# Optimization experiments

Measured on AMD Instinct MI355X. Metric: run time of the kernel, lower is better.

Reference implementation:

```python
import jax, jax.numpy as jnp
import numpy as np

H = 768      # hidden_size (MambaConfig default)
DI = 500     # intermediate_size (overridden)
N = 16       # state_size
R = 48       # time_step_rank = ceil(768/16)
K = 4        # conv_kernel
LYR = 5      # num_hidden_layers
EPS = 1e-5   # layer_norm_epsilon
B, L, IN = 8, 1024, 4096


def _rmsnorm(x, w):
    v = jnp.mean(jnp.square(x), axis=-1, keepdims=True)
    return x * jax.lax.rsqrt(v + EPS) * w


def _mixer(x, in_proj, conv_w, conv_b, x_proj, dt_w, dt_b, A_log, Dp, out_w):
    # x: [B, L, H]
    proj = x @ in_proj                       # [B, L, 2*DI]
    u, gate = jnp.split(proj, 2, axis=-1)
    # causal depthwise conv1d (torch Conv1d padding=K-1, sliced to L)
    up = jnp.pad(u, ((0, 0), (K - 1, 0), (0, 0)))
    conv = conv_b
    for k in range(K):
        conv = conv + up[:, k:k + x.shape[1], :] * conv_w[:, k]
    u = jax.nn.silu(conv)                    # [B, L, DI]
    ssm = u @ x_proj                         # [B, L, R + 2N]
    dt, Bm, Cm = ssm[..., :R], ssm[..., R:R + N], ssm[..., R + N:]
    dt = jax.nn.softplus(dt @ dt_w + dt_b)   # [B, L, DI]
    A = -jnp.exp(A_log)                      # [DI, N]
    dA = jnp.exp(dt[..., None] * A)          # [B, L, DI, N]
    dBu = dt[..., None] * Bm[:, :, None, :] * u[..., None]  # [B, L, DI, N]

    def step(h, xs):
        dA_t, dBu_t, C_t = xs
        h = dA_t * h + dBu_t                 # [B, DI, N]
        y = jnp.einsum('bdn,bn->bd', h, C_t)
        return h, y

    h0 = jnp.zeros((u.shape[0], DI, N), dtype=u.dtype)
    _, ys = jax.lax.scan(step, h0, (dA.transpose(1, 0, 2, 3),
                                    dBu.transpose(1, 0, 2, 3),
                                    Cm.transpose(1, 0, 2)))
    y = ys.transpose(1, 0, 2)                # [B, L, DI]
    y = y + u * Dp
    y = y * jax.nn.silu(gate)
    return y @ out_w                         # [B, L, H]


def setup_inputs() -> dict:
    key = jax.random.key(0)
    ks = jax.random.split(key, 12)
    s = 0.02
    inputs = jax.random.normal(ks[0], (B, L, IN), jnp.float32)
    W_down = jax.random.normal(ks[1], (IN, H), jnp.float32) * s
    in_proj = jax.random.normal(ks[2], (LYR, H, 2 * DI), jnp.float32) * s
    conv_w = jax.random.normal(ks[3], (LYR, DI, K), jnp.float32) * 0.1
    conv_b = jnp.zeros((LYR, DI), jnp.float32)
    x_proj = jax.random.normal(ks[4], (LYR, DI, R + 2 * N), jnp.float32) * s
    dt_w = jax.random.normal(ks[5], (LYR, R, DI), jnp.float32) * s
    dt_b = jax.random.normal(ks[6], (LYR, DI), jnp.float32) * 0.1
    A_log = jnp.broadcast_to(jnp.log(jnp.arange(1, N + 1, dtype=jnp.float32)),
                             (LYR, DI, N)).copy()
    D_param = jnp.ones((LYR, DI), jnp.float32)
    out_w = jax.random.normal(ks[7], (LYR, DI, H), jnp.float32) * s
    norm_w = jnp.ones((LYR, H), jnp.float32)
    norm_f_w = jnp.ones((H,), jnp.float32)
    W_cls = jax.random.normal(ks[8], (H, 1), jnp.float32) * s
    return dict(inputs=inputs, W_down=W_down, in_proj=in_proj, conv_w=conv_w,
                conv_b=conv_b, x_proj=x_proj, dt_w=dt_w, dt_b=dt_b,
                A_log=A_log, D_param=D_param, out_w=out_w, norm_w=norm_w,
                norm_f_w=norm_f_w, W_cls=W_cls)


def reference(inputs, W_down, in_proj, conv_w, conv_b, x_proj, dt_w, dt_b,
              A_log, D_param, out_w, norm_w, norm_f_w, W_cls):
    x = inputs @ W_down                      # down projection [B, L, H]
    for i in range(LYR):
        x = x + _mixer(_rmsnorm(x, norm_w[i]), in_proj[i], conv_w[i],
                       conv_b[i], x_proj[i], dt_w[i], dt_b[i], A_log[i],
                       D_param[i], out_w[i])
    x = _rmsnorm(x, norm_f_w)
    out = x[:, -1]                           # last token [B, H]
    logits = out @ W_cls                     # [B, 1]
    return logits
```

## Files before the change

kernel.cpp:

```cpp
#include <hip/hip_runtime.h>
#include <hip/hip_bf16.h>

#define BATCH 8
#define SEQL 1024
#define INDIM 4096
#define HDIM 768
#define DI 500
#define NSTATE 16
#define RRANK 48
#define KCONV 4
#define NLAYER 5
#define BL (BATCH * SEQL)

typedef __attribute__((ext_vector_type(8))) short bf16x8;
typedef __attribute__((ext_vector_type(4))) float f32x4;

__device__ __forceinline__ void gl_lds16(const void* g, void* l) {
  __builtin_amdgcn_global_load_lds(
      (const __attribute__((address_space(1))) void*)g,
      (__attribute__((address_space(3))) void*)l, 16, 0, 0);
}

__device__ __forceinline__ unsigned short f2bf(float v) {
  return __hip_bfloat16_raw(__float2bfloat16(v)).x;
}
__device__ __forceinline__ float bf2f(unsigned short h) {
  unsigned int u = ((unsigned int)h) << 16;
  float f;
  memcpy(&f, &u, 4);
  return f;
}

template <int EPI>
__global__ __launch_bounds__(256) void gemm_mfma(
    const short* __restrict__ A, const short* __restrict__ Bt,
    float* __restrict__ C, const float* __restrict__ bias,
    unsigned short* __restrict__ D0, unsigned short* __restrict__ D1,
    int M, int N, int K, int lda, int ldb, int ldc) {
  __shared__ short As[3][128 * 32];
  __shared__ short Bs[3][128 * 32];
  const int tid = threadIdx.x;
  const int w = tid >> 6, lane = tid & 63;

  const int gx = gridDim.x;
  const int nwg = gx * gridDim.y;
  int flat = blockIdx.y * gx + blockIdx.x;
  flat = (flat & 7) * (nwg >> 3) + (flat >> 3);
  const int m0 = (flat / gx) * 128, n0 = (flat % gx) * 128;

  const int wr = w >> 1, wc = w & 1;
  f32x4 acc[4][4] = {};

  const int srow = tid >> 2;
  const int cpos = tid & 3;
  const int sc = (cpos ^ ((srow >> 1) & 3)) * 8;
  const short* ga0 = A + (size_t)(m0 + srow) * lda + sc;
  const short* ga1 = A + (size_t)(m0 + 64 + srow) * lda + sc;
  const short* gb0 = Bt + (size_t)(n0 + srow) * ldb + sc;
  const short* gb1 = Bt + (size_t)(n0 + 64 + srow) * ldb + sc;
  const int lr = lane & 15, kb = lane >> 4;
  const int kbx = (kb ^ ((lr >> 1) & 3)) * 8;

  auto stage = [&](int buf, int k0) {
    gl_lds16(ga0 + k0, &As[buf][w * 512]);
    gl_lds16(ga1 + k0, &As[buf][2048 + w * 512]);
    gl_lds16(gb0 + k0, &Bs[buf][w * 512]);
    gl_lds16(gb1 + k0, &Bs[buf][2048 + w * 512]);
  };
  auto compute = [&](int buf) {
    bf16x8 af[4], bfr[4];
#pragma unroll
    for (int i = 0; i < 4; ++i) {
      af[i] = *(const bf16x8*)&As[buf][(wr * 64 + i * 16 + lr) * 32 + kbx];
      bfr[i] = *(const bf16x8*)&Bs[buf][(wc * 64 + i * 16 + lr) * 32 + kbx];
    }
#pragma unroll
    for (int i = 0; i < 4; ++i)
#pragma unroll
      for (int j = 0; j < 4; ++j)
        acc[i][j] = __builtin_amdgcn_mfma_f32_16x16x32_bf16(af[i], bfr[j],
                                                            acc[i][j], 0, 0, 0);
  };

  const int nk = K >> 5;
  stage(0, 0);
  if (nk > 1) stage(1, 32);
  int cur = 0;
  for (int t = 0; t < nk; ++t) {
    if (t + 1 < nk)
      asm volatile("s_waitcnt vmcnt(4)" ::: "memory");
    else
      asm volatile("s_waitcnt vmcnt(0)" ::: "memory");
    __builtin_amdgcn_s_barrier();
    __builtin_amdgcn_sched_barrier(0);
    compute(cur);
    if (t + 2 < nk) {
      int nb = cur + 2;
      if (nb >= 3) nb -= 3;
      stage(nb, (t + 2) * 32);
    }
    ++cur;
    if (cur == 3) cur = 0;
  }

#pragma unroll
  for (int i = 0; i < 4; ++i) {
    const int row = m0 + wr * 64 + i * 16 + (lane >> 4) * 4;
#pragma unroll
    for (int j = 0; j < 4; ++j) {
      const int col = n0 + wc * 64 + j * 16 + (lane & 15);
      if (EPI == 3) {
        if (col < N) {
          float4 v4;
#pragma unroll
          for (int r = 0; r < 4; ++r) {
            float v = acc[i][j][r] + bias[col];
            ((float*)&v4)[r] = (v > 15.f) ? v : log1pf(expf(v));
          }
          const int bb = row >> 10, tt = row & 1023;
          *(float4*)&C[((size_t)bb * DI + col) * 1024 + tt] = v4;
        }
      } else if (EPI == 4) {
#pragma unroll
        for (int r = 0; r < 4; ++r) {
          unsigned short h = f2bf(acc[i][j][r]);
          size_t rr = (size_t)(row + r);
          if (col < DI)
            D0[rr * 512 + col] = h;
          else
            D1[rr * 512 + (col - DI)] = h;
        }
      } else if (EPI == 5) {
#pragma unroll
        for (int r = 0; r < 4; ++r) {
          float v = acc[i][j][r];
          size_t rr = (size_t)(row + r);
          if (col < N) C[rr * ldc + col] = v;
          if (col < 64) D0[rr * 64 + col] = f2bf(col < RRANK ? v : 0.f);
        }
      } else {
        if (col < N) {
#pragma unroll
          for (int r = 0; r < 4; ++r) {
            float v = acc[i][j][r];
            size_t idx = (size_t)(row + r) * ldc + col;
            if (EPI == 1) v += C[idx];
            C[idx] = v;
          }
        }
      }
    }
  }
}

__global__ __launch_bounds__(256) void convert_cast(
    const float* __restrict__ src, __hip_bfloat16* __restrict__ dst, long n) {
  long i = ((long)blockIdx.x * 256 + threadIdx.x) * 4;
  if (i >= n) return;
  float4 v = *(const float4*)(src + i);
  dst[i + 0] = __float2bfloat16(v.x);
  dst[i + 1] = __float2bfloat16(v.y);
  dst[i + 2] = __float2bfloat16(v.z);
  dst[i + 3] = __float2bfloat16(v.w);
}

__global__ __launch_bounds__(256) void convert_wT(
    const float* __restrict__ src, __hip_bfloat16* __restrict__ dst, int K,
    int N, int Kpad, int Npad, long src_lstride, long dst_lstride) {
  int idx = blockIdx.x * 256 + threadIdx.x;
  int per = Kpad * Npad;
  if (idx >= per) return;
  const float* s = src + (long)blockIdx.y * src_lstride;
  __hip_bfloat16* d = dst + (long)blockIdx.y * dst_lstride;
  int n = idx / Kpad, k = idx % Kpad;
  float v = (k < K && n < N) ? s[(long)k * N + n] : 0.f;
  d[idx] = __float2bfloat16(v);
}

__device__ __forceinline__ float block_sum256(float v, float* sm) {
#pragma unroll
  for (int off = 32; off > 0; off >>= 1) v += __shfl_down(v, off, 64);
  int wid = threadIdx.x >> 6;
  if ((threadIdx.x & 63) == 0) sm[wid] = v;
  __syncthreads();
  float t = sm[0] + sm[1] + sm[2] + sm[3];
  __syncthreads();
  return t;
}

__global__ __launch_bounds__(256) void rmsnorm_kernel(
    const float* __restrict__ X, const float* __restrict__ w,
    __hip_bfloat16* __restrict__ XN) {
  __shared__ float sm[4];
  const long row = blockIdx.x;
  const float* x = X + row * HDIM;
  float vals[3];
  float s = 0.f;
#pragma unroll
  for (int j = 0; j < 3; ++j) {
    vals[j] = x[threadIdx.x + j * 256];
    s += vals[j] * vals[j];
  }
  float tot = block_sum256(s, sm);
  float scale = rsqrtf(tot / (float)HDIM + 1e-5f);
#pragma unroll
  for (int j = 0; j < 3; ++j) {
    int c = threadIdx.x + j * 256;
    XN[row * HDIM + c] = __float2bfloat16(vals[j] * scale * w[c]);
  }
}

__global__ __launch_bounds__(256) void conv_fused_kernel(
    const unsigned short* __restrict__ Uraw, const float* __restrict__ cw,
    const float* __restrict__ cb, unsigned short* __restrict__ Ubf,
    unsigned short* __restrict__ Ut, int layer) {
  __shared__ unsigned short tin[35][33];
  __shared__ unsigned short tout[32][33];
  const int d0 = blockIdx.x * 32, t0 = blockIdx.y * 32, b = blockIdx.z;
  const int tx = threadIdx.x & 31, ty = threadIdx.x >> 5;
#pragma unroll
  for (int r = 0; r < 5; ++r) {
    int tr = ty + r * 8;
    if (tr < 35) {
      int t = t0 + tr - (KCONV - 1);
      tin[tr][tx] =
          (t >= 0) ? Uraw[((size_t)b * 1024 + t) * 512 + d0 + tx] : 0;
    }
  }
  __syncthreads();
  const int d = d0 + tx;
  float w0 = 0.f, w1 = 0.f, w2 = 0.f, w3 = 0.f, bias = 0.f;
  if (d < DI) {
    const float* w = cw + ((size_t)layer * DI + d) * KCONV;
    w0 = w[0]; w1 = w[1]; w2 = w[2]; w3 = w[3];
    bias = cb[layer * DI + d];
  }
#pragma unroll
  for (int r = 0; r < 4; ++r) {
    const int tt = ty + r * 8;
    unsigned short h = 0;
    if (d < DI) {
      float a = bias + w0 * bf2f(tin[tt][tx]) + w1 * bf2f(tin[tt + 1][tx]) +
                w2 * bf2f(tin[tt + 2][tx]) + w3 * bf2f(tin[tt + 3][tx]);
      h = f2bf(a / (1.f + expf(-a)));
    }
    tout[tt][tx] = h;
    Ubf[((size_t)b * 1024 + t0 + tt) * 512 + d] = h;
  }
  __syncthreads();
#pragma unroll
  for (int r = 0; r < 4; ++r) {
    const int dd = ty + r * 8;
    Ut[((size_t)b * 512 + d0 + dd) * 1024 + t0 + tx] = tout[tx][dd];
  }
}

__global__ __launch_bounds__(256) void y_gate_kernel(
    const unsigned short* __restrict__ Yt, const unsigned short* __restrict__ G,
    unsigned short* __restrict__ Ybf) {
  __shared__ unsigned short tile[32][33];
  const int d0 = blockIdx.x * 32, t0 = blockIdx.y * 32, b = blockIdx.z;
  const int tx = threadIdx.x & 31, ty = threadIdx.x >> 5;
#pragma unroll
  for (int r = 0; r < 4; ++r) {
    int d = d0 + ty + r * 8;
    tile[ty + r * 8][tx] =
        (d < DI) ? Yt[((size_t)b * 512 + d) * 1024 + t0 + tx]
                 : (unsigned short)0;
  }
  __syncthreads();
#pragma unroll
  for (int r = 0; r < 4; ++r) {
    size_t row = (size_t)b * 1024 + t0 + ty + r * 8;
    int d = d0 + tx;
    float yv = 0.f;
    if (d < DI) {
      float y = bf2f(tile[tx][ty + r * 8]);
      float g = bf2f(G[row * 512 + d]);
      yv = y * (g / (1.f + expf(-g)));
    }
    Ybf[row * 512 + d] = f2bf(yv);
  }
}

__global__ __launch_bounds__(256) void scan_kernel(
    const float* __restrict__ DTt, const unsigned short* __restrict__ Ut,
    const float* __restrict__ SSM, const float* __restrict__ A_log,
    const float* __restrict__ Dparam, unsigned short* __restrict__ Yt,
    int layer) {
  __shared__ float sdt[1040];
  __shared__ float su[1040];
  __shared__ float s_ap[16][17];
  __shared__ float s_h0[16][17];
  __shared__ float s_hi[16][17];
  const int orig = blockIdx.x;
  const int blk = (orig & 7) * (BATCH * DI / 8) + (orig >> 3);
  const int b = blk / DI, d = blk % DI;
  const int tid = threadIdx.x;
  const int c = tid >> 4, n = tid & 15;

  const float* dtp = DTt + ((size_t)b * DI + d) * 1024;
  const unsigned short* up = Ut + ((size_t)b * 512 + d) * 1024;
#pragma unroll
  for (int k = 0; k < 4; ++k) {
    int x = tid + k * 256;
    sdt[x + (x >> 6)] = dtp[x];
    su[x + (x >> 6)] = bf2f(up[x]);
  }
  __syncthreads();

  const float An = -expf(A_log[((size_t)layer * DI + d) * NSTATE + n]);
  const float Dp = Dparam[layer * DI + d];
  const int t0 = c * 64;
  const int sb = t0 + c;
  const float* ssmB = SSM + ((size_t)b * 1024 + t0) * 128 + RRANK + n;

  float h = 0.f, ap = 1.f;
  for (int s = 0; s < 64; ++s) {
    float dt = sdt[sb + s];
    float a = __expf(dt * An);
    h = a * h + dt * su[sb + s] * ssmB[(size_t)s * 128];
    ap *= a;
  }
  s_ap[c][n] = ap;
  s_h0[c][n] = h;
  __syncthreads();

  if (tid < 16) {
    float hi = 0.f;
    for (int cc = 0; cc < 16; ++cc) {
      s_hi[cc][tid] = hi;
      hi = s_ap[cc][tid] * hi + s_h0[cc][tid];
    }
  }
  __syncthreads();

  h = s_hi[c][n];
  unsigned short* yp = Yt + ((size_t)b * 512 + d) * 1024 + t0;
  for (int s = 0; s < 64; ++s) {
    float dt = sdt[sb + s];
    float u = su[sb + s];
    float a = __expf(dt * An);
    h = a * h + dt * u * ssmB[(size_t)s * 128];
    float p = h * ssmB[(size_t)s * 128 + 16];
    p += __shfl_xor(p, 1, 64);
    p += __shfl_xor(p, 2, 64);
    p += __shfl_xor(p, 4, 64);
    p += __shfl_xor(p, 8, 64);
    if (n == 0) {
      float y = p + u * Dp;
      yp[s] = f2bf(y);
    }
  }
}

__global__ __launch_bounds__(256) void final_kernel(
    const float* __restrict__ X, const float* __restrict__ nfw,
    const float* __restrict__ Wcls, float* __restrict__ out) {
  __shared__ float sm[4];
  const int b = blockIdx.x;
  const long row = (long)b * SEQL + (SEQL - 1);
  const float* x = X + row * HDIM;
  float vals[3];
  float s = 0.f;
#pragma unroll
  for (int j = 0; j < 3; ++j) {
    vals[j] = x[threadIdx.x + j * 256];
    s += vals[j] * vals[j];
  }
  float tot = block_sum256(s, sm);
  float scale = rsqrtf(tot / (float)HDIM + 1e-5f);
  float dot = 0.f;
#pragma unroll
  for (int j = 0; j < 3; ++j) {
    int c = threadIdx.x + j * 256;
    dot += vals[j] * scale * nfw[c] * Wcls[c];
  }
  float td = block_sum256(dot, sm);
  if (threadIdx.x == 0) out[b] = td;
}

extern "C" void kernel_launch(void* const* d_in, const int* in_sizes, int n_in,
                              void* d_out, int out_size, void* d_ws,
                              size_t ws_size, hipStream_t stream) {
  const float* inputs  = (const float*)d_in[0];
  const float* W_down  = (const float*)d_in[1];
  const float* in_proj = (const float*)d_in[2];
  const float* conv_w  = (const float*)d_in[3];
  const float* conv_b  = (const float*)d_in[4];
  const float* x_proj  = (const float*)d_in[5];
  const float* dt_w    = (const float*)d_in[6];
  const float* dt_b    = (const float*)d_in[7];
  const float* A_log   = (const float*)d_in[8];
  const float* D_param = (const float*)d_in[9];
  const float* out_w   = (const float*)d_in[10];
  const float* norm_w  = (const float*)d_in[11];
  const float* norm_fw = (const float*)d_in[12];
  const float* W_cls   = (const float*)d_in[13];
  float* out = (float*)d_out;

  char* ws = (char*)d_ws;
  __hip_bfloat16* Abf   = (__hip_bfloat16*)(ws + 0);
  __hip_bfloat16* Wdbf  = (__hip_bfloat16*)(ws + 67108864);
  __hip_bfloat16* XNbf  = (__hip_bfloat16*)(ws + 0);
  unsigned short* Yt    = (unsigned short*)(ws + 0);
  float*          DTt   = (float*)(ws + 12582912);
  unsigned short* Uraw  = (unsigned short*)(ws + 28966912);
  unsigned short* Ybf   = (unsigned short*)(ws + 28966912);
  unsigned short* Gate  = (unsigned short*)(ws + 37355520);
  unsigned short* Ubf   = (unsigned short*)(ws + 45744128);
  unsigned short* Ut    = (unsigned short*)(ws + 54132736);
  float*          SSM   = (float*)(ws + 62521344);
  __hip_bfloat16* SSMbf = (__hip_bfloat16*)(ws + 66715648);
  float*          X     = (float*)(ws + 73400320);
  __hip_bfloat16* inpbf = (__hip_bfloat16*)(ws + 98566144);
  __hip_bfloat16* xpbf  = (__hip_bfloat16*)(ws + 106430464);
  __hip_bfloat16* dtwbf = (__hip_bfloat16*)(ws + 107085824);
  __hip_bfloat16* outwbf= (__hip_bfloat16*)(ws + 107413504);

  convert_cast<<<(long)BL * 4096 / 4 / 256, 256, 0, stream>>>(inputs, Abf,
                                                              (long)BL * 4096);
  convert_wT<<<dim3((768 * 4096 + 255) / 256, 1), 256, 0, stream>>>(
      W_down, Wdbf, 4096, 768, 4096, 768, 0, 0);
  convert_wT<<<dim3((768 * 1024 + 255) / 256, NLAYER), 256, 0, stream>>>(
      in_proj, inpbf, 768, 1000, 768, 1024, (long)HDIM * 1000, 768 * 1024);
  convert_wT<<<dim3((128 * 512 + 255) / 256, NLAYER), 256, 0, stream>>>(
      x_proj, xpbf, 500, 80, 512, 128, (long)DI * 80, 128 * 512);
  convert_wT<<<dim3((512 * 64 + 255) / 256, NLAYER), 256, 0, stream>>>(
      dt_w, dtwbf, 48, 500, 64, 512, (long)RRANK * DI, 512 * 64);
  convert_wT<<<dim3((768 * 512 + 255) / 256, NLAYER), 256, 0, stream>>>(
      out_w, outwbf, 500, 768, 512, 768, (long)DI * HDIM, 768 * 512);

  gemm_mfma<0><<<dim3(768 / 128, BL / 128), 256, 0, stream>>>(
      (const short*)Abf, (const short*)Wdbf, X, nullptr, nullptr, nullptr, BL,
      HDIM, INDIM, INDIM, INDIM, HDIM);

  for (int i = 0; i < NLAYER; ++i) {
    rmsnorm_kernel<<<BL, 256, 0, stream>>>(X, norm_w + i * HDIM, XNbf);
    gemm_mfma<4><<<dim3(1024 / 128, BL / 128), 256, 0, stream>>>(
        (const short*)XNbf, (const short*)(inpbf + (long)i * 768 * 1024),
        nullptr, nullptr, Uraw, Gate, BL, 1000, HDIM, HDIM, HDIM, 0);
    conv_fused_kernel<<<dim3(16, 32, 8), 256, 0, stream>>>(Uraw, conv_w,
                                                           conv_b, Ubf, Ut, i);
    gemm_mfma<5><<<dim3(1, BL / 128), 256, 0, stream>>>(
        (const short*)Ubf, (const short*)(xpbf + (long)i * 128 * 512), SSM,
        nullptr, (unsigned short*)SSMbf, nullptr, BL, 80, 512, 512, 512, 128);
    gemm_mfma<3><<<dim3(512 / 128, BL / 128), 256, 0, stream>>>(
        (const short*)SSMbf, (const short*)(dtwbf + (long)i * 512 * 64), DTt,
        dt_b + i * DI, nullptr, nullptr, BL, DI, 64, 64, 64, 0);
    scan_kernel<<<BATCH * DI, 256, 0, stream>>>(DTt, Ut, SSM, A_log, D_param,
                                                Yt, i);
    y_gate_kernel<<<dim3(16, 32, 8), 256, 0, stream>>>(Yt, Gate, Ybf);
    gemm_mfma<1><<<dim3(768 / 128, BL / 128), 256, 0, stream>>>(
        (const short*)Ybf, (const short*)(outwbf + (long)i * 768 * 512), X,
        nullptr, nullptr, nullptr, BL, HDIM, 512, 512, 512, HDIM);
  }

  final_kernel<<<BATCH, 256, 0, stream>>>(X, norm_fw, W_cls, out);
}
```

Baseline: 1.158 ms.

## Restructure selective scan: 32 chunks, interleaved B/C layout, DPP reductions

```diff
diff --git a/kernel.cpp b/kernel.cpp
--- a/kernel.cpp
+++ b/kernel.cpp
@@ -29,6 +29,13 @@
   float f;
   memcpy(&f, &u, 4);
   return f;
+}
+
+template <int CTRL>
+__device__ __forceinline__ float ror_add(float x) {
+  int r = __builtin_amdgcn_update_dpp(0, __float_as_int(x), CTRL, 0xf, 0xf,
+                                      true);
+  return x + __int_as_float(r);
 }
 
 template <int EPI>
@@ -135,8 +142,9 @@
         for (int r = 0; r < 4; ++r) {
           float v = acc[i][j][r];
           size_t rr = (size_t)(row + r);
-          if (col < N) C[rr * ldc + col] = v;
           if (col < 64) D0[rr * 64 + col] = f2bf(col < RRANK ? v : 0.f);
+          if (col >= RRANK && col < 64) C[rr * 32 + 2 * (col - RRANK)] = v;
+          if (col >= 64 && col < 80) C[rr * 32 + 2 * (col - 64) + 1] = v;
         }
       } else {
         if (col < N) {
@@ -283,16 +291,15 @@
   }
 }
 
-__global__ __launch_bounds__(256) void scan_kernel(
+__global__ __launch_bounds__(512) void scan_kernel(
     const float* __restrict__ DTt, const unsigned short* __restrict__ Ut,
-    const float* __restrict__ SSM, const float* __restrict__ A_log,
+    const float* __restrict__ BC, const float* __restrict__ A_log,
     const float* __restrict__ Dparam, unsigned short* __restrict__ Yt,
     int layer) {
-  __shared__ float sdt[1040];
-  __shared__ float su[1040];
-  __shared__ float s_ap[16][17];
-  __shared__ float s_h0[16][17];
-  __shared__ float s_hi[16][17];
+  __shared__ float2 sdtu[1056];
+  __shared__ float s_ap[32][17];
+  __shared__ float s_h0[32][17];
+  __shared__ float s_hi[32][17];
   const int orig = blockIdx.x;
   const int blk = (orig & 7) * (BATCH * DI / 8) + (orig >> 3);
   const int b = blk / DI, d = blk % DI;
@@ -302,24 +309,25 @@
   const float* dtp = DTt + ((size_t)b * DI + d) * 1024;
   const unsigned short* up = Ut + ((size_t)b * 512 + d) * 1024;
 #pragma unroll
-  for (int k = 0; k < 4; ++k) {
-    int x = tid + k * 256;
-    sdt[x + (x >> 6)] = dtp[x];
-    su[x + (x >> 6)] = bf2f(up[x]);
-  }
-  __syncthreads();
-
-  const float An = -expf(A_log[((size_t)layer * DI + d) * NSTATE + n]);
+  for (int k = 0; k < 2; ++k) {
+    int x = tid + k * 512;
+    sdtu[x + (x >> 5)] = make_float2(dtp[x], bf2f(up[x]));
+  }
+  __syncthreads();
+
+  const float An2 =
+      -expf(A_log[((size_t)layer * DI + d) * NSTATE + n]) * 1.44269504f;
   const float Dp = Dparam[layer * DI + d];
-  const int t0 = c * 64;
-  const int sb = t0 + c;
-  const float* ssmB = SSM + ((size_t)b * 1024 + t0) * 128 + RRANK + n;
+  const int t0 = c * 32;
+  const float2* sb = sdtu + c * 33;
+  const float2* bc = (const float2*)(BC + ((size_t)b * 1024 + t0) * 32) + n;
 
   float h = 0.f, ap = 1.f;
-  for (int s = 0; s < 64; ++s) {
-    float dt = sdt[sb + s];
-    float a = __expf(dt * An);
-    h = a * h + dt * su[sb + s] * ssmB[(size_t)s * 128];
+#pragma unroll 4
+  for (int s = 0; s < 32; ++s) {
+    float2 du = sb[s];
+    float a = exp2f(du.x * An2);
+    h = a * h + du.x * du.y * bc[s * 16].x;
     ap *= a;
   }
   s_ap[c][n] = ap;
@@ -328,7 +336,7 @@
 
   if (tid < 16) {
     float hi = 0.f;
-    for (int cc = 0; cc < 16; ++cc) {
+    for (int cc = 0; cc < 32; ++cc) {
       s_hi[cc][tid] = hi;
       hi = s_ap[cc][tid] * hi + s_h0[cc][tid];
     }
@@ -337,19 +345,19 @@
 
   h = s_hi[c][n];
   unsigned short* yp = Yt + ((size_t)b * 512 + d) * 1024 + t0;
-  for (int s = 0; s < 64; ++s) {
-    float dt = sdt[sb + s];
-    float u = su[sb + s];
-    float a = __expf(dt * An);
-    h = a * h + dt * u * ssmB[(size_t)s * 128];
-    float p = h * ssmB[(size_t)s * 128 + 16];
-    p += __shfl_xor(p, 1, 64);
-    p += __shfl_xor(p, 2, 64);
-    p += __shfl_xor(p, 4, 64);
-    p += __shfl_xor(p, 8, 64);
+#pragma unroll 4
+  for (int s = 0; s < 32; ++s) {
+    float2 du = sb[s];
+    float2 v = bc[s * 16];
+    float a = exp2f(du.x * An2);
+    h = a * h + du.x * du.y * v.x;
+    float p = h * v.y;
+    p = ror_add<0x128>(p);
+    p = ror_add<0x124>(p);
+    p = ror_add<0x122>(p);
+    p = ror_add<0x121>(p);
     if (n == 0) {
-      float y = p + u * Dp;
-      yp[s] = f2bf(y);
+      yp[s] = f2bf(p + du.y * Dp);
     }
   }
 }
@@ -410,7 +418,7 @@
   unsigned short* Gate  = (unsigned short*)(ws + 37355520);
   unsigned short* Ubf   = (unsigned short*)(ws + 45744128);
   unsigned short* Ut    = (unsigned short*)(ws + 54132736);
-  float*          SSM   = (float*)(ws + 62521344);
+  float*          BC    = (float*)(ws + 62521344);
   __hip_bfloat16* SSMbf = (__hip_bfloat16*)(ws + 66715648);
   float*          X     = (float*)(ws + 73400320);
   __hip_bfloat16* inpbf = (__hip_bfloat16*)(ws + 98566144);
@@ -443,12 +451,12 @@
     conv_fused_kernel<<<dim3(16, 32, 8), 256, 0, stream>>>(Uraw, conv_w,
                                                            conv_b, Ubf, Ut, i);
     gemm_mfma<5><<<dim3(1, BL / 128), 256, 0, stream>>>(
-        (const short*)Ubf, (const short*)(xpbf + (long)i * 128 * 512), SSM,
-        nullptr, (unsigned short*)SSMbf, nullptr, BL, 80, 512, 512, 512, 128);
+        (const short*)Ubf, (const short*)(xpbf + (long)i * 128 * 512), BC,
+        nullptr, (unsigned short*)SSMbf, nullptr, BL, 80, 512, 512, 512, 0);
     gemm_mfma<3><<<dim3(512 / 128, BL / 128), 256, 0, stream>>>(
         (const short*)SSMbf, (const short*)(dtwbf + (long)i * 512 * 64), DTt,
         dt_b + i * DI, nullptr, nullptr, BL, DI, 64, 64, 64, 0);
-    scan_kernel<<<BATCH * DI, 256, 0, stream>>>(DTt, Ut, SSM, A_log, D_param,
+    scan_kernel<<<BATCH * DI, 512, 0, stream>>>(DTt, Ut, BC, A_log, D_param,
                                                 Yt, i);
     y_gate_kernel<<<dim3(16, 32, 8), 256, 0, stream>>>(Yt, Gate, Ybf);
     gemm_mfma<1><<<dim3(768 / 128, BL / 128), 256, 0, stream>>>(
```

Result: no change. 1.137 ms (-1.8%).
